# Kernel tuning notes

Measured on AMD Instinct MI355X. Metric: run time of the kernel, lower is better.

## Reference

```python
import jax, jax.numpy as jnp
import numpy as np

DROP_PERCENT = 0.25


def setup_inputs() -> dict:
    key = jax.random.key(0)
    k1, k2, k3 = jax.random.split(key, 3)
    B, D, C = 16384, 4096, 1000
    x = jax.random.normal(k1, (B, D), dtype=jnp.float32)
    prev_output = jax.random.normal(k2, (B, C), dtype=jnp.float32)
    weight_matrix = jax.random.normal(k3, (C, D), dtype=jnp.float32)
    return {"x": x, "prev_output": prev_output, "weight_matrix": weight_matrix}


def reference(x, prev_output, weight_matrix):
    # top-2 predicted classes per row: [B, 2]
    _, top_ind = jax.lax.top_k(prev_output, 2)
    # gather the two corresponding classifier weight rows: [B, 2, D]
    sel = weight_matrix[top_ind]
    # difference of the two class weight vectors: [B, D]
    diffs = sel[:, 0, :] - sel[:, 1, :]
    # channel confusion scores
    scores = jnp.abs(x * diffs)
    num_dropped = int(x.shape[1] * DROP_PERCENT)
    # indices of the top-scoring channels to drop: [B, num_dropped]
    _, dropped = jax.lax.top_k(scores, num_dropped)
    rows = jnp.arange(x.shape[0])[:, None]  # [B, 1]
    mask = jnp.ones(x.shape, dtype=bool).at[rows, dropped].set(False)
    return x * mask
```

## Files before the change

kernel.cpp:

```cpp
#include <hip/hip_runtime.h>
#include <cstdint>
#include <cstddef>

constexpr int Dn    = 4096;
constexpr int Cn    = 1000;
constexpr int NDROP = 1024;
constexpr int TPB   = 256;

__device__ __forceinline__ unsigned long long pack_pv(float v, unsigned idx) {
  unsigned b = __float_as_uint(v);
  unsigned u = b ^ ((b & 0x80000000u) ? 0xFFFFFFFFu : 0x80000000u);
  return ((unsigned long long)u << 32) | (unsigned)(~idx);
}

__global__ __launch_bounds__(TPB) void ConfusionDropout_52407190946399_kernel(
    const float* __restrict__ x,
    const float* __restrict__ prev,
    const float* __restrict__ W,
    float* __restrict__ out)
{
  const int row  = blockIdx.x;
  const int t    = threadIdx.x;
  const int wave = t >> 6;

  __shared__ unsigned long long s_a0[TPB];
  __shared__ unsigned long long s_a1[TPB];
  __shared__ unsigned s_cnt[2][4];
  __shared__ unsigned s_cnt2[2][4];
  __shared__ unsigned s_scan[TPB];

  unsigned long long a0 = 0ull, a1 = 0ull;
  {
    const float* pr = prev + (size_t)row * Cn;
    #pragma unroll
    for (int k = 0; k < 4; ++k) {
      int c = t + k * TPB;
      if (c < Cn) {
        unsigned long long p = pack_pv(pr[c], (unsigned)c);
        if (p > a0)      { a1 = a0; a0 = p; }
        else if (p > a1) { a1 = p; }
      }
    }
  }
  s_a0[t] = a0; s_a1[t] = a1;
  __syncthreads();
  for (int s = TPB / 2; s > 0; s >>= 1) {
    if (t < s) {
      unsigned long long b0 = s_a0[t + s], b1 = s_a1[t + s];
      unsigned long long c0 = s_a0[t],     c1 = s_a1[t];
      unsigned long long n0, n1;
      if (b0 > c0) { n0 = b0; n1 = (c0 > b1) ? c0 : b1; }
      else         { n0 = c0; n1 = (b0 > c1) ? b0 : c1; }
      s_a0[t] = n0; s_a1[t] = n1;
    }
    __syncthreads();
  }
  const unsigned i0 = ~(unsigned)(s_a0[0] & 0xFFFFFFFFull);
  const unsigned i1 = ~(unsigned)(s_a1[0] & 0xFFFFFFFFull);

  const float* xr = x + (size_t)row * Dn;
  const float* w0 = W + (size_t)i0 * Dn;
  const float* w1 = W + (size_t)i1 * Dn;

  float    xv[16];
  unsigned key[16];
  #pragma unroll
  for (int j = 0; j < 4; ++j) {
    const int d4 = t * 16 + j * 4;
    float4 xx = *reinterpret_cast<const float4*>(xr + d4);
    float4 aa = *reinterpret_cast<const float4*>(w0 + d4);
    float4 bb = *reinterpret_cast<const float4*>(w1 + d4);
    xv[j*4+0] = xx.x; xv[j*4+1] = xx.y; xv[j*4+2] = xx.z; xv[j*4+3] = xx.w;
    key[j*4+0] = __float_as_uint(xx.x * (aa.x - bb.x)) & 0x7FFFFFFFu;
    key[j*4+1] = __float_as_uint(xx.y * (aa.y - bb.y)) & 0x7FFFFFFFu;
    key[j*4+2] = __float_as_uint(xx.z * (aa.z - bb.z)) & 0x7FFFFFFFu;
    key[j*4+3] = __float_as_uint(xx.w * (aa.w - bb.w)) & 0x7FFFFFFFu;
  }

  unsigned cur = 0;
  #pragma unroll 1
  for (int bit = 30; bit >= 0; --bit) {
    const unsigned cand = cur | (1u << bit);
    unsigned wc = 0;
    #pragma unroll
    for (int j = 0; j < 16; ++j)
      wc += (unsigned)__popcll(__ballot(key[j] >= cand));
    if ((t & 63) == 0) s_cnt[bit & 1][wave] = wc;
    __syncthreads();
    const unsigned tot = s_cnt[bit & 1][0] + s_cnt[bit & 1][1] +
                         s_cnt[bit & 1][2] + s_cnt[bit & 1][3];
    if (tot >= NDROP) cur = cand;
  }
  const unsigned V = cur;

  unsigned wgt = 0, weq = 0;
  #pragma unroll
  for (int j = 0; j < 16; ++j) {
    wgt += (unsigned)__popcll(__ballot(key[j] > V));
    weq += (unsigned)__popcll(__ballot(key[j] == V));
  }
  if ((t & 63) == 0) { s_cnt2[0][wave] = wgt; s_cnt2[1][wave] = weq; }
  __syncthreads();
  const unsigned cnt_gt  = s_cnt2[0][0] + s_cnt2[0][1] + s_cnt2[0][2] + s_cnt2[0][3];
  const unsigned cnt_eq  = s_cnt2[1][0] + s_cnt2[1][1] + s_cnt2[1][2] + s_cnt2[1][3];
  const unsigned need_eq = NDROP - cnt_gt;

  bool drop[16];
  if (need_eq == cnt_eq) {
    #pragma unroll
    for (int j = 0; j < 16; ++j) drop[j] = (key[j] >= V);
  } else {
    unsigned c = 0;
    #pragma unroll
    for (int j = 0; j < 16; ++j) c += (key[j] == V) ? 1u : 0u;
    s_scan[t] = c;
    __syncthreads();
    for (int off = 1; off < TPB; off <<= 1) {
      unsigned add = (t >= off) ? s_scan[t - off] : 0u;
      __syncthreads();
      s_scan[t] += add;
      __syncthreads();
    }
    unsigned run = s_scan[t] - c;
    #pragma unroll
    for (int j = 0; j < 16; ++j) {
      if (key[j] == V) { drop[j] = (run < need_eq); ++run; }
      else             { drop[j] = (key[j] > V); }
    }
  }

  float* orow = out + (size_t)row * Dn + t * 16;
  #pragma unroll
  for (int j = 0; j < 4; ++j) {
    float4 o;
    o.x = drop[j*4+0] ? 0.0f : xv[j*4+0];
    o.y = drop[j*4+1] ? 0.0f : xv[j*4+1];
    o.z = drop[j*4+2] ? 0.0f : xv[j*4+2];
    o.w = drop[j*4+3] ? 0.0f : xv[j*4+3];
    *reinterpret_cast<float4*>(orow + j * 4) = o;
  }
}

extern "C" void kernel_launch(void* const* d_in, const int* in_sizes, int n_in,
                              void* d_out, int out_size, void* d_ws, size_t ws_size,
                              hipStream_t stream) {
  const float* x    = (const float*)d_in[0];
  const float* prev = (const float*)d_in[1];
  const float* W    = (const float*)d_in[2];
  float* out        = (float*)d_out;
  const int Brows   = in_sizes[0] / Dn;
  ConfusionDropout_52407190946399_kernel<<<Brows, TPB, 0, stream>>>(x, prev, W, out);
}
```

Before: 603.5 us.

## Process one row per wavefront, removing block-wide syncs from top-k selection

```diff
diff --git a/kernel.cpp b/kernel.cpp
--- a/kernel.cpp
+++ b/kernel.cpp
@@ -19,22 +19,17 @@
     const float* __restrict__ W,
     float* __restrict__ out)
 {
-  const int row  = blockIdx.x;
-  const int t    = threadIdx.x;
-  const int wave = t >> 6;
-
-  __shared__ unsigned long long s_a0[TPB];
-  __shared__ unsigned long long s_a1[TPB];
-  __shared__ unsigned s_cnt[2][4];
-  __shared__ unsigned s_cnt2[2][4];
-  __shared__ unsigned s_scan[TPB];
+  const int wave = threadIdx.x >> 6;
+  const int l    = threadIdx.x & 63;
+  const int row  = blockIdx.x * (TPB / 64) + wave;
+  const unsigned long long ltmask = (1ull << l) - 1ull;
 
   unsigned long long a0 = 0ull, a1 = 0ull;
   {
     const float* pr = prev + (size_t)row * Cn;
     #pragma unroll
-    for (int k = 0; k < 4; ++k) {
-      int c = t + k * TPB;
+    for (int k = 0; k < 16; ++k) {
+      int c = l + k * 64;
       if (c < Cn) {
         unsigned long long p = pack_pv(pr[c], (unsigned)c);
         if (p > a0)      { a1 = a0; a0 = p; }
@@ -42,102 +37,94 @@
       }
     }
   }
-  s_a0[t] = a0; s_a1[t] = a1;
-  __syncthreads();
-  for (int s = TPB / 2; s > 0; s >>= 1) {
-    if (t < s) {
-      unsigned long long b0 = s_a0[t + s], b1 = s_a1[t + s];
-      unsigned long long c0 = s_a0[t],     c1 = s_a1[t];
-      unsigned long long n0, n1;
-      if (b0 > c0) { n0 = b0; n1 = (c0 > b1) ? c0 : b1; }
-      else         { n0 = c0; n1 = (b0 > c1) ? b0 : c1; }
-      s_a0[t] = n0; s_a1[t] = n1;
-    }
-    __syncthreads();
+  #pragma unroll
+  for (int off = 1; off < 64; off <<= 1) {
+    unsigned long long b0 = __shfl_xor(a0, off, 64);
+    unsigned long long b1 = __shfl_xor(a1, off, 64);
+    if (b0 > a0) { a1 = (a0 > b1) ? a0 : b1; a0 = b0; }
+    else         { a1 = (b0 > a1) ? b0 : a1; }
   }
-  const unsigned i0 = ~(unsigned)(s_a0[0] & 0xFFFFFFFFull);
-  const unsigned i1 = ~(unsigned)(s_a1[0] & 0xFFFFFFFFull);
+  const unsigned i0 = ~(unsigned)(a0 & 0xFFFFFFFFull);
+  const unsigned i1 = ~(unsigned)(a1 & 0xFFFFFFFFull);
 
-  const float* xr = x + (size_t)row * Dn;
-  const float* w0 = W + (size_t)i0 * Dn;
-  const float* w1 = W + (size_t)i1 * Dn;
+  const float* xr   = x   + (size_t)row * Dn + l * 4;
+  const float* w0   = W   + (size_t)i0  * Dn + l * 4;
+  const float* w1   = W   + (size_t)i1  * Dn + l * 4;
+  float*       orow = out + (size_t)row * Dn + l * 4;
 
-  float    xv[16];
-  unsigned key[16];
+  unsigned key[64];
   #pragma unroll
-  for (int j = 0; j < 4; ++j) {
-    const int d4 = t * 16 + j * 4;
-    float4 xx = *reinterpret_cast<const float4*>(xr + d4);
-    float4 aa = *reinterpret_cast<const float4*>(w0 + d4);
-    float4 bb = *reinterpret_cast<const float4*>(w1 + d4);
-    xv[j*4+0] = xx.x; xv[j*4+1] = xx.y; xv[j*4+2] = xx.z; xv[j*4+3] = xx.w;
-    key[j*4+0] = __float_as_uint(xx.x * (aa.x - bb.x)) & 0x7FFFFFFFu;
-    key[j*4+1] = __float_as_uint(xx.y * (aa.y - bb.y)) & 0x7FFFFFFFu;
-    key[j*4+2] = __float_as_uint(xx.z * (aa.z - bb.z)) & 0x7FFFFFFFu;
-    key[j*4+3] = __float_as_uint(xx.w * (aa.w - bb.w)) & 0x7FFFFFFFu;
+  for (int k = 0; k < 16; ++k) {
+    float4 xx = *reinterpret_cast<const float4*>(xr + k * 256);
+    float4 aa = *reinterpret_cast<const float4*>(w0 + k * 256);
+    float4 bb = *reinterpret_cast<const float4*>(w1 + k * 256);
+    key[k*4+0] = __float_as_uint(xx.x * (aa.x - bb.x)) & 0x7FFFFFFFu;
+    key[k*4+1] = __float_as_uint(xx.y * (aa.y - bb.y)) & 0x7FFFFFFFu;
+    key[k*4+2] = __float_as_uint(xx.z * (aa.z - bb.z)) & 0x7FFFFFFFu;
+    key[k*4+3] = __float_as_uint(xx.w * (aa.w - bb.w)) & 0x7FFFFFFFu;
+    *reinterpret_cast<float4*>(orow + k * 256) = xx;
   }
 
   unsigned cur = 0;
   #pragma unroll 1
   for (int bit = 30; bit >= 0; --bit) {
     const unsigned cand = cur | (1u << bit);
-    unsigned wc = 0;
+    unsigned cnt = 0;
     #pragma unroll
-    for (int j = 0; j < 16; ++j)
-      wc += (unsigned)__popcll(__ballot(key[j] >= cand));
-    if ((t & 63) == 0) s_cnt[bit & 1][wave] = wc;
-    __syncthreads();
-    const unsigned tot = s_cnt[bit & 1][0] + s_cnt[bit & 1][1] +
-                         s_cnt[bit & 1][2] + s_cnt[bit & 1][3];
-    if (tot >= NDROP) cur = cand;
+    for (int j = 0; j < 64; ++j)
+      cnt += (unsigned)__popcll(__ballot(key[j] >= cand));
+    if (cnt >= NDROP) cur = cand;
   }
   const unsigned V = cur;
 
-  unsigned wgt = 0, weq = 0;
+  unsigned cnt_gt = 0, cnt_eq = 0;
   #pragma unroll
-  for (int j = 0; j < 16; ++j) {
-    wgt += (unsigned)__popcll(__ballot(key[j] > V));
-    weq += (unsigned)__popcll(__ballot(key[j] == V));
+  for (int j = 0; j < 64; ++j) {
+    cnt_gt += (unsigned)__popcll(__ballot(key[j] >  V));
+    cnt_eq += (unsigned)__popcll(__ballot(key[j] == V));
   }
-  if ((t & 63) == 0) { s_cnt2[0][wave] = wgt; s_cnt2[1][wave] = weq; }
-  __syncthreads();
-  const unsigned cnt_gt  = s_cnt2[0][0] + s_cnt2[0][1] + s_cnt2[0][2] + s_cnt2[0][3];
-  const unsigned cnt_eq  = s_cnt2[1][0] + s_cnt2[1][1] + s_cnt2[1][2] + s_cnt2[1][3];
   const unsigned need_eq = NDROP - cnt_gt;
 
-  bool drop[16];
+  unsigned long long dropmask = 0ull;
   if (need_eq == cnt_eq) {
     #pragma unroll
-    for (int j = 0; j < 16; ++j) drop[j] = (key[j] >= V);
+    for (int j = 0; j < 64; ++j)
+      if (key[j] >= V) dropmask |= (1ull << j);
   } else {
-    unsigned c = 0;
+    unsigned base = 0;
     #pragma unroll
-    for (int j = 0; j < 16; ++j) c += (key[j] == V) ? 1u : 0u;
-    s_scan[t] = c;
-    __syncthreads();
-    for (int off = 1; off < TPB; off <<= 1) {
-      unsigned add = (t >= off) ? s_scan[t - off] : 0u;
-      __syncthreads();
-      s_scan[t] += add;
-      __syncthreads();
-    }
-    unsigned run = s_scan[t] - c;
-    #pragma unroll
-    for (int j = 0; j < 16; ++j) {
-      if (key[j] == V) { drop[j] = (run < need_eq); ++run; }
-      else             { drop[j] = (key[j] > V); }
+    for (int k = 0; k < 16; ++k) {
+      unsigned long long bm0 = __ballot(key[k*4+0] == V);
+      unsigned long long bm1 = __ballot(key[k*4+1] == V);
+      unsigned long long bm2 = __ballot(key[k*4+2] == V);
+      unsigned long long bm3 = __ballot(key[k*4+3] == V);
+      unsigned beforeL = (unsigned)__popcll(bm0 & ltmask) + (unsigned)__popcll(bm1 & ltmask)
+                       + (unsigned)__popcll(bm2 & ltmask) + (unsigned)__popcll(bm3 & ltmask);
+      unsigned sameLane = 0;
+      #pragma unroll
+      for (int m = 0; m < 4; ++m) {
+        const int j = k * 4 + m;
+        if (key[j] == V) {
+          unsigned rank = base + beforeL + sameLane;
+          if (rank < need_eq) dropmask |= (1ull << j);
+          ++sameLane;
+        } else if (key[j] > V) {
+          dropmask |= (1ull << j);
+        }
+      }
+      base += (unsigned)__popcll(bm0) + (unsigned)__popcll(bm1)
+            + (unsigned)__popcll(bm2) + (unsigned)__popcll(bm3);
     }
   }
 
-  float* orow = out + (size_t)row * Dn + t * 16;
+  asm volatile("s_waitcnt vmcnt(0)" ::: "memory");
   #pragma unroll
-  for (int j = 0; j < 4; ++j) {
-    float4 o;
-    o.x = drop[j*4+0] ? 0.0f : xv[j*4+0];
-    o.y = drop[j*4+1] ? 0.0f : xv[j*4+1];
-    o.z = drop[j*4+2] ? 0.0f : xv[j*4+2];
-    o.w = drop[j*4+3] ? 0.0f : xv[j*4+3];
-    *reinterpret_cast<float4*>(orow + j * 4) = o;
+  for (int k = 0; k < 16; ++k) {
+    #pragma unroll
+    for (int m = 0; m < 4; ++m) {
+      if ((dropmask >> (k * 4 + m)) & 1ull)
+        orow[k * 256 + m] = 0.0f;
+    }
   }
 }
 
@@ -149,5 +136,5 @@
   const float* W    = (const float*)d_in[2];
   float* out        = (float*)d_out;
   const int Brows   = in_sizes[0] / Dn;
-  ConfusionDropout_52407190946399_kernel<<<Brows, TPB, 0, stream>>>(x, prev, W, out);
+  ConfusionDropout_52407190946399_kernel<<<Brows / (TPB / 64), TPB, 0, stream>>>(x, prev, W, out);
 }
```

Measured after the change: 677.0 us. 12.2% more time.

## Prefetch x row before top-2 and use wave shuffles for top-2 reduction

Applied to the files above, without the earlier changes.

```diff
diff --git a/kernel.cpp b/kernel.cpp
--- a/kernel.cpp
+++ b/kernel.cpp
@@ -13,69 +13,93 @@
   return ((unsigned long long)u << 32) | (unsigned)(~idx);
 }
 
-__global__ __launch_bounds__(TPB) void ConfusionDropout_52407190946399_kernel(
+__global__ __launch_bounds__(TPB, 4) void ConfusionDropout_52407190946399_kernel(
     const float* __restrict__ x,
     const float* __restrict__ prev,
     const float* __restrict__ W,
     float* __restrict__ out)
 {
-  const int row  = blockIdx.x;
   const int t    = threadIdx.x;
   const int wave = t >> 6;
+  const int row  = blockIdx.x;
 
-  __shared__ unsigned long long s_a0[TPB];
-  __shared__ unsigned long long s_a1[TPB];
+  __shared__ unsigned long long s_top[4][2];
   __shared__ unsigned s_cnt[2][4];
   __shared__ unsigned s_cnt2[2][4];
   __shared__ unsigned s_scan[TPB];
 
+  const float* xr = x + (size_t)row * Dn + t * 16;
+  const float4 xx0 = *reinterpret_cast<const float4*>(xr + 0);
+  const float4 xx1 = *reinterpret_cast<const float4*>(xr + 4);
+  const float4 xx2 = *reinterpret_cast<const float4*>(xr + 8);
+  const float4 xx3 = *reinterpret_cast<const float4*>(xr + 12);
+
+  const float* pr = prev + (size_t)row * Cn;
+  float pv0 = 0.f, pv1 = 0.f, pv2 = 0.f, pv3 = 0.f;
+  const bool g3 = (t + 768) < Cn;
+  pv0 = pr[t];
+  pv1 = pr[t + 256];
+  pv2 = pr[t + 512];
+  if (g3) pv3 = pr[t + 768];
+
   unsigned long long a0 = 0ull, a1 = 0ull;
   {
-    const float* pr = prev + (size_t)row * Cn;
+    unsigned long long p;
+    p = pack_pv(pv0, (unsigned)t);                    if (p > a0) { a1 = a0; a0 = p; } else if (p > a1) a1 = p;
+    p = pack_pv(pv1, (unsigned)(t + 256));            if (p > a0) { a1 = a0; a0 = p; } else if (p > a1) a1 = p;
+    p = pack_pv(pv2, (unsigned)(t + 512));            if (p > a0) { a1 = a0; a0 = p; } else if (p > a1) a1 = p;
+    if (g3) { p = pack_pv(pv3, (unsigned)(t + 768));  if (p > a0) { a1 = a0; a0 = p; } else if (p > a1) a1 = p; }
+  }
+  #pragma unroll
+  for (int off = 1; off < 64; off <<= 1) {
+    unsigned long long b0 = __shfl_xor(a0, off, 64);
+    unsigned long long b1 = __shfl_xor(a1, off, 64);
+    if (b0 > a0) { a1 = (a0 > b1) ? a0 : b1; a0 = b0; }
+    else         { a1 = (b0 > a1) ? b0 : a1; }
+  }
+  if ((t & 63) == 0) { s_top[wave][0] = a0; s_top[wave][1] = a1; }
+  __syncthreads();
+  {
+    unsigned long long m0 = s_top[0][0], m1 = s_top[0][1];
     #pragma unroll
-    for (int k = 0; k < 4; ++k) {
-      int c = t + k * TPB;
-      if (c < Cn) {
-        unsigned long long p = pack_pv(pr[c], (unsigned)c);
-        if (p > a0)      { a1 = a0; a0 = p; }
-        else if (p > a1) { a1 = p; }
-      }
+    for (int w = 1; w < 4; ++w) {
+      unsigned long long b0 = s_top[w][0], b1 = s_top[w][1];
+      if (b0 > m0) { m1 = (m0 > b1) ? m0 : b1; m0 = b0; }
+      else         { m1 = (b0 > m1) ? b0 : m1; }
     }
+    a0 = m0; a1 = m1;
   }
-  s_a0[t] = a0; s_a1[t] = a1;
-  __syncthreads();
-  for (int s = TPB / 2; s > 0; s >>= 1) {
-    if (t < s) {
-      unsigned long long b0 = s_a0[t + s], b1 = s_a1[t + s];
-      unsigned long long c0 = s_a0[t],     c1 = s_a1[t];
-      unsigned long long n0, n1;
-      if (b0 > c0) { n0 = b0; n1 = (c0 > b1) ? c0 : b1; }
-      else         { n0 = c0; n1 = (b0 > c1) ? b0 : c1; }
-      s_a0[t] = n0; s_a1[t] = n1;
-    }
-    __syncthreads();
-  }
-  const unsigned i0 = ~(unsigned)(s_a0[0] & 0xFFFFFFFFull);
-  const unsigned i1 = ~(unsigned)(s_a1[0] & 0xFFFFFFFFull);
+  const unsigned i0 = ~(unsigned)(a0 & 0xFFFFFFFFull);
+  const unsigned i1 = ~(unsigned)(a1 & 0xFFFFFFFFull);
 
-  const float* xr = x + (size_t)row * Dn;
-  const float* w0 = W + (size_t)i0 * Dn;
-  const float* w1 = W + (size_t)i1 * Dn;
+  const float* w0 = W + (size_t)i0 * Dn + t * 16;
+  const float* w1 = W + (size_t)i1 * Dn + t * 16;
+  const float4 aa0 = *reinterpret_cast<const float4*>(w0 + 0);
+  const float4 aa1 = *reinterpret_cast<const float4*>(w0 + 4);
+  const float4 aa2 = *reinterpret_cast<const float4*>(w0 + 8);
+  const float4 aa3 = *reinterpret_cast<const float4*>(w0 + 12);
+  const float4 bb0 = *reinterpret_cast<const float4*>(w1 + 0);
+  const float4 bb1 = *reinterpret_cast<const float4*>(w1 + 4);
+  const float4 bb2 = *reinterpret_cast<const float4*>(w1 + 8);
+  const float4 bb3 = *reinterpret_cast<const float4*>(w1 + 12);
 
-  float    xv[16];
   unsigned key[16];
-  #pragma unroll
-  for (int j = 0; j < 4; ++j) {
-    const int d4 = t * 16 + j * 4;
-    float4 xx = *reinterpret_cast<const float4*>(xr + d4);
-    float4 aa = *reinterpret_cast<const float4*>(w0 + d4);
-    float4 bb = *reinterpret_cast<const float4*>(w1 + d4);
-    xv[j*4+0] = xx.x; xv[j*4+1] = xx.y; xv[j*4+2] = xx.z; xv[j*4+3] = xx.w;
-    key[j*4+0] = __float_as_uint(xx.x * (aa.x - bb.x)) & 0x7FFFFFFFu;
-    key[j*4+1] = __float_as_uint(xx.y * (aa.y - bb.y)) & 0x7FFFFFFFu;
-    key[j*4+2] = __float_as_uint(xx.z * (aa.z - bb.z)) & 0x7FFFFFFFu;
-    key[j*4+3] = __float_as_uint(xx.w * (aa.w - bb.w)) & 0x7FFFFFFFu;
-  }
+  key[ 0] = __float_as_uint(xx0.x * (aa0.x - bb0.x)) & 0x7FFFFFFFu;
+  key[ 1] = __float_as_uint(xx0.y * (aa0.y - bb0.y)) & 0x7FFFFFFFu;
+  key[ 2] = __float_as_uint(xx0.z * (aa0.z - bb0.z)) & 0x7FFFFFFFu;
+  key[ 3] = __float_as_uint(xx0.w * (aa0.w - bb0.w)) & 0x7FFFFFFFu;
+  key[ 4] = __float_as_uint(xx1.x * (aa1.x - bb1.x)) & 0x7FFFFFFFu;
+  key[ 5] = __float_as_uint(xx1.y * (aa1.y - bb1.y)) & 0x7FFFFFFFu;
+  key[ 6] = __float_as_uint(xx1.z * (aa1.z - bb1.z)) & 0x7FFFFFFFu;
+  key[ 7] = __float_as_uint(xx1.w * (aa1.w - bb1.w)) & 0x7FFFFFFFu;
+  key[ 8] = __float_as_uint(xx2.x * (aa2.x - bb2.x)) & 0x7FFFFFFFu;
+  key[ 9] = __float_as_uint(xx2.y * (aa2.y - bb2.y)) & 0x7FFFFFFFu;
+  key[10] = __float_as_uint(xx2.z * (aa2.z - bb2.z)) & 0x7FFFFFFFu;
+  key[11] = __float_as_uint(xx2.w * (aa2.w - bb2.w)) & 0x7FFFFFFFu;
+  key[12] = __float_as_uint(xx3.x * (aa3.x - bb3.x)) & 0x7FFFFFFFu;
+  key[13] = __float_as_uint(xx3.y * (aa3.y - bb3.y)) & 0x7FFFFFFFu;
+  key[14] = __float_as_uint(xx3.z * (aa3.z - bb3.z)) & 0x7FFFFFFFu;
+  key[15] = __float_as_uint(xx3.w * (aa3.w - bb3.w)) & 0x7FFFFFFFu;
 
   unsigned cur = 0;
   #pragma unroll 1
@@ -96,7 +120,7 @@
   unsigned wgt = 0, weq = 0;
   #pragma unroll
   for (int j = 0; j < 16; ++j) {
-    wgt += (unsigned)__popcll(__ballot(key[j] > V));
+    wgt += (unsigned)__popcll(__ballot(key[j] >  V));
     weq += (unsigned)__popcll(__ballot(key[j] == V));
   }
   if ((t & 63) == 0) { s_cnt2[0][wave] = wgt; s_cnt2[1][wave] = weq; }
@@ -130,15 +154,19 @@
   }
 
   float* orow = out + (size_t)row * Dn + t * 16;
-  #pragma unroll
-  for (int j = 0; j < 4; ++j) {
-    float4 o;
-    o.x = drop[j*4+0] ? 0.0f : xv[j*4+0];
-    o.y = drop[j*4+1] ? 0.0f : xv[j*4+1];
-    o.z = drop[j*4+2] ? 0.0f : xv[j*4+2];
-    o.w = drop[j*4+3] ? 0.0f : xv[j*4+3];
-    *reinterpret_cast<float4*>(orow + j * 4) = o;
-  }
+  float4 o0 = xx0, o1 = xx1, o2 = xx2, o3 = xx3;
+  if (drop[ 0]) o0.x = 0.0f;  if (drop[ 1]) o0.y = 0.0f;
+  if (drop[ 2]) o0.z = 0.0f;  if (drop[ 3]) o0.w = 0.0f;
+  if (drop[ 4]) o1.x = 0.0f;  if (drop[ 5]) o1.y = 0.0f;
+  if (drop[ 6]) o1.z = 0.0f;  if (drop[ 7]) o1.w = 0.0f;
+  if (drop[ 8]) o2.x = 0.0f;  if (drop[ 9]) o2.y = 0.0f;
+  if (drop[10]) o2.z = 0.0f;  if (drop[11]) o2.w = 0.0f;
+  if (drop[12]) o3.x = 0.0f;  if (drop[13]) o3.y = 0.0f;
+  if (drop[14]) o3.z = 0.0f;  if (drop[15]) o3.w = 0.0f;
+  *reinterpret_cast<float4*>(orow + 0)  = o0;
+  *reinterpret_cast<float4*>(orow + 4)  = o1;
+  *reinterpret_cast<float4*>(orow + 8)  = o2;
+  *reinterpret_cast<float4*>(orow + 12) = o3;
 }
 
 extern "C" void kernel_launch(void* const* d_in, const int* in_sizes, int n_in,
```

Result: faster. 543.3 us (-10.0%).
